# Kernel optimization log

Hardware: AMD Instinct MI355X
Metric: run time of the kernel (lower is better)

The kernel has to match this reference:

```python
import jax, jax.numpy as jnp
import numpy as np

OUT_H, OUT_W = 64, 256  # layer's output_size


def setup_inputs() -> dict:
    key = jax.random.key(0)
    k1, k2 = jax.random.split(key)
    image = jax.random.normal(k1, (32, 128, 512, 32), dtype=jnp.float32)
    theta = jax.random.normal(k2, (32, 6), dtype=jnp.float32)
    return {"image": image, "theta": theta}


def _make_grid(out_h, out_w):
    # homogeneous sampling grid in [-1, 1], shape (3, out_h*out_w)
    xs = jnp.linspace(-1.0, 1.0, out_w)
    ys = jnp.linspace(-1.0, 1.0, out_h)
    xg, yg = jnp.meshgrid(xs, ys)  # each (out_h, out_w)
    ones = jnp.ones_like(xg)
    return jnp.stack([xg.ravel(), yg.ravel(), ones.ravel()], axis=0)


def reference(image, theta):
    B, H, W, C = image.shape
    theta = theta.reshape(B, 2, 3)
    # faithful to the original's debug hack: zero row 1 of batch 0 and row 0 of batch 1
    theta = theta.at[0, 1].set(0.0).at[1, 0].set(0.0)

    grid = _make_grid(OUT_H, OUT_W)                      # (3, N)
    coords = jnp.einsum('brc,cn->brn', theta, grid)      # (B, 2, N)
    x = 0.5 * (coords[:, 0] + 1.0) * W                   # (B, N) -- note: uses W, not W-1 (as in source)
    y = 0.5 * (coords[:, 1] + 1.0) * H

    x0 = x.astype(jnp.int32)                             # truncation toward zero, matches K.cast
    y0 = y.astype(jnp.int32)
    x1, y1 = x0 + 1, y0 + 1
    x0 = jnp.clip(x0, 0, W - 1)
    x1 = jnp.clip(x1, 0, W - 1)
    y0 = jnp.clip(y0, 0, H - 1)
    y1 = jnp.clip(y1, 0, H - 1)

    flat = image.reshape(B, H * W, C)

    def gather(yy, xx):
        idx = (yy * W + xx)[..., None]                   # (B, N, 1)
        return jnp.take_along_axis(flat, idx, axis=1)    # (B, N, C)

    pA = gather(y0, x0)  # top-left
    pB = gather(y1, x0)  # bottom-left
    pC = gather(y0, x1)  # top-right
    pD = gather(y1, x1)  # bottom-right

    x0f, x1f = x0.astype(jnp.float32), x1.astype(jnp.float32)
    y0f, y1f = y0.astype(jnp.float32), y1.astype(jnp.float32)
    wA = ((x1f - x) * (y1f - y))[..., None]
    wB = ((x1f - x) * (y - y0f))[..., None]
    wC = ((x - x0f) * (y1f - y))[..., None]
    wD = ((x - x0f) * (y - y0f))[..., None]

    out = pA * wA + pB * wB + pC * wC + pD * wD          # (B, N, C)
    return out.reshape(B, OUT_H, OUT_W, C)
```

## Files before the change

### kernel.cpp

```cpp
#include <hip/hip_runtime.h>

#define BB 32
#define HH 128
#define WW 512
#define CC 32
#define OUT_H 64
#define OUT_W 256

__global__ __launch_bounds__(256) void bilin_kernel(
    const float* __restrict__ image,
    const float* __restrict__ theta,
    float* __restrict__ out)
{
    const int gid = blockIdx.x * blockDim.x + threadIdx.x;
    const int c4 = gid & 7;
    const int p  = gid >> 3;
    const int j  = p & (OUT_W - 1);
    const int i  = (p >> 8) & (OUT_H - 1);
    const int b  = p >> 14;

    float t0 = theta[b * 6 + 0];
    float t1 = theta[b * 6 + 1];
    float t2 = theta[b * 6 + 2];
    float t3 = theta[b * 6 + 3];
    float t4 = theta[b * 6 + 4];
    float t5 = theta[b * 6 + 5];
    if (b == 0) { t3 = 0.0f; t4 = 0.0f; t5 = 0.0f; }
    if (b == 1) { t0 = 0.0f; t1 = 0.0f; t2 = 0.0f; }

    const float xg = -1.0f + 2.0f * (float)j / 255.0f;
    const float yg = -1.0f + 2.0f * (float)i / 63.0f;

    const float xh = t0 * xg + t1 * yg + t2;
    const float yh = t3 * xg + t4 * yg + t5;
    const float x = 0.5f * (xh + 1.0f) * (float)WW;
    const float y = 0.5f * (yh + 1.0f) * (float)HH;

    int x0 = (int)x;
    int y0 = (int)y;
    int x1 = x0 + 1;
    int y1 = y0 + 1;
    x0 = min(max(x0, 0), WW - 1);
    x1 = min(max(x1, 0), WW - 1);
    y0 = min(max(y0, 0), HH - 1);
    y1 = min(max(y1, 0), HH - 1);

    const float x0f = (float)x0, x1f = (float)x1;
    const float y0f = (float)y0, y1f = (float)y1;
    const float wA = (x1f - x) * (y1f - y);
    const float wB = (x1f - x) * (y - y0f);
    const float wC = (x - x0f) * (y1f - y);
    const float wD = (x - x0f) * (y - y0f);

    const float4* __restrict__ img4 = (const float4*)image;
    const long long batch_base = (long long)b * (HH * WW * (CC / 4));
    const int rowA = (y0 * WW + x0) * (CC / 4) + c4;
    const int rowB = (y1 * WW + x0) * (CC / 4) + c4;
    const int rowC = (y0 * WW + x1) * (CC / 4) + c4;
    const int rowD = (y1 * WW + x1) * (CC / 4) + c4;

    const float4 pA = img4[batch_base + rowA];
    const float4 pB = img4[batch_base + rowB];
    const float4 pC = img4[batch_base + rowC];
    const float4 pD = img4[batch_base + rowD];

    float4 o;
    o.x = pA.x * wA + pB.x * wB + pC.x * wC + pD.x * wD;
    o.y = pA.y * wA + pB.y * wB + pC.y * wC + pD.y * wD;
    o.z = pA.z * wA + pB.z * wB + pC.z * wC + pD.z * wD;
    o.w = pA.w * wA + pB.w * wB + pC.w * wC + pD.w * wD;

    ((float4*)out)[gid] = o;
}

extern "C" void kernel_launch(void* const* d_in, const int* in_sizes, int n_in,
                              void* d_out, int out_size, void* d_ws, size_t ws_size,
                              hipStream_t stream) {
    const float* image = (const float*)d_in[0];
    const float* theta = (const float*)d_in[1];
    float* out = (float*)d_out;

    const int total4 = BB * OUT_H * OUT_W * (CC / 4);
    const int block = 256;
    const int grid = total4 / block;
    bilin_kernel<<<grid, block, 0, stream>>>(image, theta, out);
}
```

Measured before the change: 329.5 us.

## Process two float4 channel chunks per thread and swizzle block order across XCDs

Each thread now computes two float4 channel groups (c2 and c2+4) instead of one, halving the thread count and amortizing the per-pixel coordinate and weight math. Block IDs are remapped so contiguous output chunks land on the same XCD (blockIdx & 7 selects chunk), aiming for better L2 locality of gathered image rows. Indexing switches from 64-bit to 32-bit offsets. The trade-offs are higher register use per thread and strided (4-apart) float4 access within each pixel.

```diff
diff --git a/kernel.cpp b/kernel.cpp
--- a/kernel.cpp
+++ b/kernel.cpp
@@ -8,13 +8,15 @@
 #define OUT_W 256
 
 __global__ __launch_bounds__(256) void bilin_kernel(
-    const float* __restrict__ image,
+    const float4* __restrict__ img4,
     const float* __restrict__ theta,
-    float* __restrict__ out)
+    float4* __restrict__ out4)
 {
-    const int gid = blockIdx.x * blockDim.x + threadIdx.x;
-    const int c4 = gid & 7;
-    const int p  = gid >> 3;
+    const int chunk = gridDim.x >> 3;
+    const int bid = (blockIdx.x & 7) * chunk + (blockIdx.x >> 3);
+    const int q = bid * blockDim.x + threadIdx.x;
+    const int c2 = q & 3;
+    const int p  = q >> 2;
     const int j  = p & (OUT_W - 1);
     const int i  = (p >> 8) & (OUT_H - 1);
     const int b  = p >> 14;
@@ -52,36 +54,45 @@
     const float wC = (x - x0f) * (y1f - y);
     const float wD = (x - x0f) * (y - y0f);
 
-    const float4* __restrict__ img4 = (const float4*)image;
-    const long long batch_base = (long long)b * (HH * WW * (CC / 4));
-    const int rowA = (y0 * WW + x0) * (CC / 4) + c4;
-    const int rowB = (y1 * WW + x0) * (CC / 4) + c4;
-    const int rowC = (y0 * WW + x1) * (CC / 4) + c4;
-    const int rowD = (y1 * WW + x1) * (CC / 4) + c4;
+    const int base = b * (HH * WW * (CC / 4));
+    const int rowA = base + (y0 * WW + x0) * (CC / 4) + c2;
+    const int rowB = base + (y1 * WW + x0) * (CC / 4) + c2;
+    const int rowC = base + (y0 * WW + x1) * (CC / 4) + c2;
+    const int rowD = base + (y1 * WW + x1) * (CC / 4) + c2;
 
-    const float4 pA = img4[batch_base + rowA];
-    const float4 pB = img4[batch_base + rowB];
-    const float4 pC = img4[batch_base + rowC];
-    const float4 pD = img4[batch_base + rowD];
+    const float4 A0 = img4[rowA];
+    const float4 B0 = img4[rowB];
+    const float4 C0 = img4[rowC];
+    const float4 D0 = img4[rowD];
+    const float4 A1 = img4[rowA + 4];
+    const float4 B1 = img4[rowB + 4];
+    const float4 C1 = img4[rowC + 4];
+    const float4 D1 = img4[rowD + 4];
 
-    float4 o;
-    o.x = pA.x * wA + pB.x * wB + pC.x * wC + pD.x * wD;
-    o.y = pA.y * wA + pB.y * wB + pC.y * wC + pD.y * wD;
-    o.z = pA.z * wA + pB.z * wB + pC.z * wC + pD.z * wD;
-    o.w = pA.w * wA + pB.w * wB + pC.w * wC + pD.w * wD;
+    float4 o0, o1;
+    o0.x = A0.x * wA + B0.x * wB + C0.x * wC + D0.x * wD;
+    o0.y = A0.y * wA + B0.y * wB + C0.y * wC + D0.y * wD;
+    o0.z = A0.z * wA + B0.z * wB + C0.z * wC + D0.z * wD;
+    o0.w = A0.w * wA + B0.w * wB + C0.w * wC + D0.w * wD;
+    o1.x = A1.x * wA + B1.x * wB + C1.x * wC + D1.x * wD;
+    o1.y = A1.y * wA + B1.y * wB + C1.y * wC + D1.y * wD;
+    o1.z = A1.z * wA + B1.z * wB + C1.z * wC + D1.z * wD;
+    o1.w = A1.w * wA + B1.w * wB + C1.w * wC + D1.w * wD;
 
-    ((float4*)out)[gid] = o;
+    const int o = p * (CC / 4) + c2;
+    out4[o]     = o0;
+    out4[o + 4] = o1;
 }
 
 extern "C" void kernel_launch(void* const* d_in, const int* in_sizes, int n_in,
                               void* d_out, int out_size, void* d_ws, size_t ws_size,
                               hipStream_t stream) {
-    const float* image = (const float*)d_in[0];
+    const float4* img4 = (const float4*)d_in[0];
     const float* theta = (const float*)d_in[1];
-    float* out = (float*)d_out;
+    float4* out4 = (float4*)d_out;
 
-    const int total4 = BB * OUT_H * OUT_W * (CC / 4);
+    const int total_threads = BB * OUT_H * OUT_W * 4;
     const int block = 256;
-    const int grid = total4 / block;
-    bilin_kernel<<<grid, block, 0, stream>>>(image, theta, out);
+    const int grid = total_threads / block;
+    bilin_kernel<<<grid, block, 0, stream>>>(img4, theta, out4);
 }
```

Result: slower. 338.2 us (+2.7%).
